# Optimization experiments

Measured on AMD Instinct MI355X. Metric: run time of the kernel, lower is better.

The kernel has to match this reference:

```python
import jax, jax.numpy as jnp
import numpy as np

B, IH, IW, C = 128, 16, 16, 1024   # weighted_context NHWC; idf = IH*IW = 256
S, EMB, IDF = 32, 256, 256


def setup_inputs() -> dict:
    key = jax.random.key(0)
    k1, k2, k3 = jax.random.split(key, 3)
    return {
        "weighted_context": jax.random.normal(k1, (B, IH, IW, C), dtype=jnp.float32),
        "word_emb": jax.random.normal(k2, (B, S, EMB), dtype=jnp.float32),
        "conv_kernel": jax.random.normal(k3, (EMB, IDF), dtype=jnp.float32) * (1.0 / np.sqrt(EMB)),
        "conv_bias": jnp.zeros((IDF,), dtype=jnp.float32),
    }


def reference(weighted_context, word_emb, conv_kernel, conv_bias):
    b, ih, iw, c = weighted_context.shape
    s = word_emb.shape[1]
    # 1x1 conv over the (expanded) word embeddings == per-token linear projection
    we = jnp.einsum("bse,ei->bsi", word_emb, conv_kernel) + conv_bias  # [B, S, idf]
    wc = weighted_context.reshape(b, ih * iw, c)                        # [B, HW, C]
    # matmul(wc, we, transpose_a=True, transpose_b=True): contracts HW with idf (idf == HW)
    attn = jnp.einsum("bpc,bsp->bcs", wc, we)                           # [B, C, S]
    # reshape to [B*C, S] + softmax == softmax over last axis
    attn = jax.nn.softmax(attn, axis=-1)
    # matmul(we^T [B, idf, S], attn^T [B, S, C]) -> [B, idf, C]
    out = jnp.einsum("bsp,bcs->bpc", we, attn).reshape(b, ih, iw, c)
    return (out, attn)
```

## Files before the change

kernel.cpp:

```cpp
#include <hip/hip_runtime.h>


typedef float  f32x4  __attribute__((ext_vector_type(4)));
typedef short  bf16x8 __attribute__((ext_vector_type(8)));

namespace {
constexpr int kB = 128, kHW = 256, kC = 1024, kS = 32, kE = 256;
constexpr int TP = kHW + 8;
constexpr int WR = kS + 8;
}

__device__ inline ushort f2bf(float x) {
  unsigned u = __float_as_uint(x);
  u += 0x7fffu + ((u >> 16) & 1u);
  return (ushort)(u >> 16);
}
__device__ inline float bf2f(ushort h) { return __uint_as_float(((unsigned)h) << 16); }

#define MFMA16(A, Bf, Cv) __builtin_amdgcn_mfma_f32_16x16x32_bf16((A), (Bf), (Cv), 0, 0, 0)

__global__ __launch_bounds__(256, 2) void fused_attn_kernel(
    const float* __restrict__ wc, const float* __restrict__ emb,
    const float* __restrict__ Km, const float* __restrict__ bias,
    float* __restrict__ out, float* __restrict__ attn_out) {
  const int b    = blockIdx.y;
  const int cb   = blockIdx.x * 256;
  const int tid  = threadIdx.x;
  const int wave = tid >> 6, lane = tid & 63;
  const int lr   = lane & 15, lg = lane >> 4;

  __shared__ ushort wHT[kS][TP];
  __shared__ ushort wLT[kS][TP];
  __shared__ ushort wHp[kHW][WR];
  __shared__ ushort pHl[kHW][WR];

  const float* wcb = wc + (size_t)b * kHW * kC;
  const int c0 = cb + wave * 64;

  float avC[8], avN[8];
#pragma unroll
  for (int i = 0; i < 8; ++i)
    avC[i] = wcb[(size_t)(lg * 8 + i) * kC + c0 + lr];

  {
    const float* embb = emb + (size_t)b * kS * kE;
    f32x4 pcc[2][4];
#pragma unroll
    for (int m = 0; m < 2; ++m)
#pragma unroll
      for (int n = 0; n < 4; ++n) pcc[m][n] = (f32x4){0.f, 0.f, 0.f, 0.f};

#pragma unroll 1
    for (int kt = 0; kt < 8; ++kt) {
      bf16x8 eah[2], eal[2];
#pragma unroll
      for (int m = 0; m < 2; ++m) {
        const float* ep = embb + (size_t)(m * 16 + lr) * kE + kt * 32 + lg * 8;
        const float4 v0 = *(const float4*)ep;
        const float4 v1 = *(const float4*)(ep + 4);
        const float ev[8] = {v0.x, v0.y, v0.z, v0.w, v1.x, v1.y, v1.z, v1.w};
#pragma unroll
        for (int i = 0; i < 8; ++i) {
          const ushort h = f2bf(ev[i]);
          eah[m][i] = (short)h;
          eal[m][i] = (short)f2bf(ev[i] - bf2f(h));
        }
      }
#pragma unroll
      for (int n = 0; n < 4; ++n) {
        const int pg = wave * 64 + n * 16 + lr;
        bf16x8 kh, kl;
#pragma unroll
        for (int i = 0; i < 8; ++i) {
          const float kv = Km[(size_t)(kt * 32 + lg * 8 + i) * kHW + pg];
          const ushort h = f2bf(kv);
          kh[i] = (short)h;
          kl[i] = (short)f2bf(kv - bf2f(h));
        }
#pragma unroll
        for (int m = 0; m < 2; ++m) {
          pcc[m][n] = MFMA16(eah[m], kh, pcc[m][n]);
          pcc[m][n] = MFMA16(eah[m], kl, pcc[m][n]);
          pcc[m][n] = MFMA16(eal[m], kh, pcc[m][n]);
        }
      }
    }
#pragma unroll
    for (int n = 0; n < 4; ++n) {
      const int pg = wave * 64 + n * 16 + lr;
      const float bv = bias[pg];
#pragma unroll
      for (int m = 0; m < 2; ++m)
#pragma unroll
        for (int j = 0; j < 4; ++j) {
          const float x = pcc[m][n][j] + bv;
          const ushort h = f2bf(x);
          const ushort l = f2bf(x - bf2f(h));
          const int s = m * 16 + lg * 4 + j;
          wHT[s][pg] = h;
          wLT[s][pg] = l;
          wHp[pg][s] = h;
        }
    }
  }
  __syncthreads();

  f32x4 acc[4][2];
#pragma unroll
  for (int m = 0; m < 4; ++m)
#pragma unroll
    for (int n = 0; n < 2; ++n) acc[m][n] = (f32x4){0.f, 0.f, 0.f, 0.f};

#pragma unroll 1
  for (int kt = 0; kt < 8; ++kt) {
    bf16x8 bh[2], bl[2];
#pragma unroll
    for (int n = 0; n < 2; ++n) {
      bh[n] = *(const bf16x8*)&wHT[n * 16 + lr][kt * 32 + lg * 8];
      bl[n] = *(const bf16x8*)&wLT[n * 16 + lr][kt * 32 + lg * 8];
    }
#pragma unroll
    for (int m = 0; m < 4; ++m) {
      const int mn  = (m + 1) & 3;
      const int ktn = (m == 3) ? kt + 1 : kt;
      if (!(kt == 7 && m == 3)) {
#pragma unroll
        for (int i = 0; i < 8; ++i)
          avN[i] = wcb[(size_t)(ktn * 32 + lg * 8 + i) * kC + c0 + mn * 16 + lr];
      }
      bf16x8 ah, al;
#pragma unroll
      for (int i = 0; i < 8; ++i) {
        const ushort h = f2bf(avC[i]);
        ah[i] = (short)h;
        al[i] = (short)f2bf(avC[i] - bf2f(h));
      }
#pragma unroll
      for (int n = 0; n < 2; ++n) {
        acc[m][n] = MFMA16(ah, bh[n], acc[m][n]);
        acc[m][n] = MFMA16(ah, bl[n], acc[m][n]);
        acc[m][n] = MFMA16(al, bh[n], acc[m][n]);
      }
#pragma unroll
      for (int i = 0; i < 8; ++i) avC[i] = avN[i];
    }
  }

  float* attnb = attn_out + ((size_t)b * kC + cb) * kS;
#pragma unroll
  for (int m = 0; m < 4; ++m) {
#pragma unroll
    for (int j = 0; j < 4; ++j) {
      float v0 = acc[m][0][j], v1 = acc[m][1][j];
      float mx = fmaxf(v0, v1);
      mx = fmaxf(mx, __shfl_xor(mx, 1));
      mx = fmaxf(mx, __shfl_xor(mx, 2));
      mx = fmaxf(mx, __shfl_xor(mx, 4));
      mx = fmaxf(mx, __shfl_xor(mx, 8));
      float e0 = __expf(v0 - mx), e1 = __expf(v1 - mx);
      float sm = e0 + e1;
      sm += __shfl_xor(sm, 1); sm += __shfl_xor(sm, 2);
      sm += __shfl_xor(sm, 4); sm += __shfl_xor(sm, 8);
      const float inv = 1.f / sm;
      e0 *= inv; e1 *= inv;
      const int cL = wave * 64 + m * 16 + lg * 4 + j;
      attnb[(size_t)cL * kS + lr]      = e0;
      attnb[(size_t)cL * kS + 16 + lr] = e1;
      pHl[cL][lr]      = f2bf(e0);
      pHl[cL][16 + lr] = f2bf(e1);
    }
  }

  bf16x8 pbh[4];
#pragma unroll
  for (int n = 0; n < 4; ++n)
    pbh[n] = *(const bf16x8*)&pHl[wave * 64 + n * 16 + lr][lg * 8];

  float* outb = out + (size_t)b * kHW * kC + cb;
#pragma unroll 1
  for (int pt = 0; pt < 16; ++pt) {
    const bf16x8 ah = *(const bf16x8*)&wHp[pt * 16 + lr][lg * 8];
#pragma unroll
    for (int n = 0; n < 4; ++n) {
      f32x4 o = (f32x4){0.f, 0.f, 0.f, 0.f};
      o = MFMA16(ah, pbh[n], o);
      const int ccol = wave * 64 + n * 16 + lr;
#pragma unroll
      for (int j = 0; j < 4; ++j)
        outb[(size_t)(pt * 16 + lg * 4 + j) * kC + ccol] = o[j];
    }
  }
}

extern "C" void kernel_launch(void* const* d_in, const int* in_sizes, int n_in,
                              void* d_out, int out_size, void* d_ws, size_t ws_size,
                              hipStream_t stream) {
  const float* wc   = (const float*)d_in[0];
  const float* emb  = (const float*)d_in[1];
  const float* Km   = (const float*)d_in[2];
  const float* bias = (const float*)d_in[3];

  float* out  = (float*)d_out;
  float* attn = out + (size_t)kB * kHW * kC;

  fused_attn_kernel<<<dim3(4, kB), 256, 0, stream>>>(wc, emb, Km, bias, out, attn);
}
```

Before: 83.21 us.

## Pre-split conv kernel to bf16 hi/lo, double waves per block, restructure output GEMM

Adds a small prep kernel that converts the conv weight into transposed bf16 high/low halves in workspace, so the fused kernel stops reconverting the same weights in every block. The fused kernel now runs 512 threads (8 waves) per block, and each wave owns 32 positions and 32 channels, which halves per-wave register tiles and raises occupancy. The embedding and weight loads are software-prefetched a step ahead. The final out GEMM is reorganised so each wave writes its own rows of positions across all channels, using softmax probabilities shared through LDS after a new barrier. The cost is an extra launch, a workspace round trip, and an additional block-wide sync.

```diff
diff --git a/kernel.cpp b/kernel.cpp
--- a/kernel.cpp
+++ b/kernel.cpp
@@ -19,10 +19,21 @@
 
 #define MFMA16(A, Bf, Cv) __builtin_amdgcn_mfma_f32_16x16x32_bf16((A), (Bf), (Cv), 0, 0, 0)
 
-__global__ __launch_bounds__(256, 2) void fused_attn_kernel(
+__global__ __launch_bounds__(256) void km_prep_kernel(
+    const float* __restrict__ Km, ushort* __restrict__ kh,
+    ushort* __restrict__ kl) {
+  const int p = blockIdx.x, e = threadIdx.x;
+  const float v = Km[(size_t)e * kHW + p];
+  const ushort h = f2bf(v);
+  kh[(size_t)p * kE + e] = h;
+  kl[(size_t)p * kE + e] = (ushort)f2bf(v - bf2f(h));
+}
+
+__global__ __launch_bounds__(512, 4) void fused_attn_kernel(
     const float* __restrict__ wc, const float* __restrict__ emb,
-    const float* __restrict__ Km, const float* __restrict__ bias,
-    float* __restrict__ out, float* __restrict__ attn_out) {
+    const ushort* __restrict__ kmh, const ushort* __restrict__ kml,
+    const float* __restrict__ bias, float* __restrict__ out,
+    float* __restrict__ attn_out) {
   const int b    = blockIdx.y;
   const int cb   = blockIdx.x * 256;
   const int tid  = threadIdx.x;
@@ -35,30 +46,53 @@
   __shared__ ushort pHl[kHW][WR];
 
   const float* wcb = wc + (size_t)b * kHW * kC;
-  const int c0 = cb + wave * 64;
-
-  float avC[8], avN[8];
-#pragma unroll
-  for (int i = 0; i < 8; ++i)
-    avC[i] = wcb[(size_t)(lg * 8 + i) * kC + c0 + lr];
+  const int c0 = cb + wave * 32;
+  const int p0 = wave * 32;
 
   {
     const float* embb = emb + (size_t)b * kS * kE;
-    f32x4 pcc[2][4];
+    f32x4 pcc[2][2];
 #pragma unroll
     for (int m = 0; m < 2; ++m)
 #pragma unroll
-      for (int n = 0; n < 4; ++n) pcc[m][n] = (f32x4){0.f, 0.f, 0.f, 0.f};
+      for (int n = 0; n < 2; ++n) pcc[m][n] = (f32x4){0.f, 0.f, 0.f, 0.f};
+
+    float4 eC[2][2]; bf16x8 khC[2], klC[2];
+#pragma unroll
+    for (int m = 0; m < 2; ++m) {
+      const float* ep = embb + (size_t)(m * 16 + lr) * kE + lg * 8;
+      eC[m][0] = *(const float4*)ep;
+      eC[m][1] = *(const float4*)(ep + 4);
+    }
+#pragma unroll
+    for (int n = 0; n < 2; ++n) {
+      const int pg = p0 + n * 16 + lr;
+      khC[n] = *(const bf16x8*)&kmh[(size_t)pg * kE + lg * 8];
+      klC[n] = *(const bf16x8*)&kml[(size_t)pg * kE + lg * 8];
+    }
 
 #pragma unroll 1
     for (int kt = 0; kt < 8; ++kt) {
+      float4 eN[2][2]; bf16x8 khN[2], klN[2];
+      if (kt < 7) {
+        const int ko = (kt + 1) * 32;
+#pragma unroll
+        for (int m = 0; m < 2; ++m) {
+          const float* ep = embb + (size_t)(m * 16 + lr) * kE + ko + lg * 8;
+          eN[m][0] = *(const float4*)ep;
+          eN[m][1] = *(const float4*)(ep + 4);
+        }
+#pragma unroll
+        for (int n = 0; n < 2; ++n) {
+          const int pg = p0 + n * 16 + lr;
+          khN[n] = *(const bf16x8*)&kmh[(size_t)pg * kE + ko + lg * 8];
+          klN[n] = *(const bf16x8*)&kml[(size_t)pg * kE + ko + lg * 8];
+        }
+      }
       bf16x8 eah[2], eal[2];
 #pragma unroll
       for (int m = 0; m < 2; ++m) {
-        const float* ep = embb + (size_t)(m * 16 + lr) * kE + kt * 32 + lg * 8;
-        const float4 v0 = *(const float4*)ep;
-        const float4 v1 = *(const float4*)(ep + 4);
-        const float ev[8] = {v0.x, v0.y, v0.z, v0.w, v1.x, v1.y, v1.z, v1.w};
+        const float* ev = (const float*)&eC[m][0];
 #pragma unroll
         for (int i = 0; i < 8; ++i) {
           const ushort h = f2bf(ev[i]);
@@ -67,27 +101,23 @@
         }
       }
 #pragma unroll
-      for (int n = 0; n < 4; ++n) {
-        const int pg = wave * 64 + n * 16 + lr;
-        bf16x8 kh, kl;
-#pragma unroll
-        for (int i = 0; i < 8; ++i) {
-          const float kv = Km[(size_t)(kt * 32 + lg * 8 + i) * kHW + pg];
-          const ushort h = f2bf(kv);
-          kh[i] = (short)h;
-          kl[i] = (short)f2bf(kv - bf2f(h));
-        }
+      for (int n = 0; n < 2; ++n)
 #pragma unroll
         for (int m = 0; m < 2; ++m) {
-          pcc[m][n] = MFMA16(eah[m], kh, pcc[m][n]);
-          pcc[m][n] = MFMA16(eah[m], kl, pcc[m][n]);
-          pcc[m][n] = MFMA16(eal[m], kh, pcc[m][n]);
-        }
-      }
-    }
-#pragma unroll
-    for (int n = 0; n < 4; ++n) {
-      const int pg = wave * 64 + n * 16 + lr;
+          pcc[m][n] = MFMA16(eah[m], khC[n], pcc[m][n]);
+          pcc[m][n] = MFMA16(eah[m], klC[n], pcc[m][n]);
+          pcc[m][n] = MFMA16(eal[m], khC[n], pcc[m][n]);
+        }
+      if (kt < 7) {
+#pragma unroll
+        for (int m = 0; m < 2; ++m) { eC[m][0] = eN[m][0]; eC[m][1] = eN[m][1]; }
+#pragma unroll
+        for (int n = 0; n < 2; ++n) { khC[n] = khN[n]; klC[n] = klN[n]; }
+      }
+    }
+#pragma unroll
+    for (int n = 0; n < 2; ++n) {
+      const int pg = p0 + n * 16 + lr;
       const float bv = bias[pg];
 #pragma unroll
       for (int m = 0; m < 2; ++m)
@@ -95,19 +125,26 @@
         for (int j = 0; j < 4; ++j) {
           const float x = pcc[m][n][j] + bv;
           const ushort h = f2bf(x);
-          const ushort l = f2bf(x - bf2f(h));
           const int s = m * 16 + lg * 4 + j;
           wHT[s][pg] = h;
-          wLT[s][pg] = l;
+          wLT[s][pg] = (ushort)f2bf(x - bf2f(h));
           wHp[pg][s] = h;
         }
     }
   }
+
+  float avC[2][8], avN[2][8];
+#pragma unroll
+  for (int m = 0; m < 2; ++m)
+#pragma unroll
+    for (int i = 0; i < 8; ++i)
+      avC[m][i] = wcb[(size_t)(lg * 8 + i) * kC + c0 + m * 16 + lr];
+
   __syncthreads();
 
-  f32x4 acc[4][2];
-#pragma unroll
-  for (int m = 0; m < 4; ++m)
+  f32x4 acc[2][2];
+#pragma unroll
+  for (int m = 0; m < 2; ++m)
 #pragma unroll
     for (int n = 0; n < 2; ++n) acc[m][n] = (f32x4){0.f, 0.f, 0.f, 0.f};
 
@@ -119,21 +156,21 @@
       bh[n] = *(const bf16x8*)&wHT[n * 16 + lr][kt * 32 + lg * 8];
       bl[n] = *(const bf16x8*)&wLT[n * 16 + lr][kt * 32 + lg * 8];
     }
-#pragma unroll
-    for (int m = 0; m < 4; ++m) {
-      const int mn  = (m + 1) & 3;
-      const int ktn = (m == 3) ? kt + 1 : kt;
-      if (!(kt == 7 && m == 3)) {
+    if (kt < 7) {
+#pragma unroll
+      for (int m = 0; m < 2; ++m)
 #pragma unroll
         for (int i = 0; i < 8; ++i)
-          avN[i] = wcb[(size_t)(ktn * 32 + lg * 8 + i) * kC + c0 + mn * 16 + lr];
-      }
+          avN[m][i] = wcb[(size_t)((kt + 1) * 32 + lg * 8 + i) * kC + c0 + m * 16 + lr];
+    }
+#pragma unroll
+    for (int m = 0; m < 2; ++m) {
       bf16x8 ah, al;
 #pragma unroll
       for (int i = 0; i < 8; ++i) {
-        const ushort h = f2bf(avC[i]);
+        const ushort h = f2bf(avC[m][i]);
         ah[i] = (short)h;
-        al[i] = (short)f2bf(avC[i] - bf2f(h));
+        al[i] = (short)f2bf(avC[m][i] - bf2f(h));
       }
 #pragma unroll
       for (int n = 0; n < 2; ++n) {
@@ -141,14 +178,18 @@
         acc[m][n] = MFMA16(ah, bl[n], acc[m][n]);
         acc[m][n] = MFMA16(al, bh[n], acc[m][n]);
       }
-#pragma unroll
-      for (int i = 0; i < 8; ++i) avC[i] = avN[i];
+    }
+    if (kt < 7) {
+#pragma unroll
+      for (int m = 0; m < 2; ++m)
+#pragma unroll
+        for (int i = 0; i < 8; ++i) avC[m][i] = avN[m][i];
     }
   }
 
   float* attnb = attn_out + ((size_t)b * kC + cb) * kS;
 #pragma unroll
-  for (int m = 0; m < 4; ++m) {
+  for (int m = 0; m < 2; ++m) {
 #pragma unroll
     for (int j = 0; j < 4; ++j) {
       float v0 = acc[m][0][j], v1 = acc[m][1][j];
@@ -163,32 +204,35 @@
       sm += __shfl_xor(sm, 4); sm += __shfl_xor(sm, 8);
       const float inv = 1.f / sm;
       e0 *= inv; e1 *= inv;
-      const int cL = wave * 64 + m * 16 + lg * 4 + j;
+      const int cL = wave * 32 + m * 16 + lg * 4 + j;
       attnb[(size_t)cL * kS + lr]      = e0;
       attnb[(size_t)cL * kS + 16 + lr] = e1;
       pHl[cL][lr]      = f2bf(e0);
       pHl[cL][16 + lr] = f2bf(e1);
     }
   }
-
-  bf16x8 pbh[4];
-#pragma unroll
-  for (int n = 0; n < 4; ++n)
-    pbh[n] = *(const bf16x8*)&pHl[wave * 64 + n * 16 + lr][lg * 8];
-
+  __syncthreads();
+
+  const bf16x8 ahB0 = *(const bf16x8*)&wHp[p0 + lr][lg * 8];
+  const bf16x8 ahB1 = *(const bf16x8*)&wHp[p0 + 16 + lr][lg * 8];
   float* outb = out + (size_t)b * kHW * kC + cb;
+
+  bf16x8 pbC = *(const bf16x8*)&pHl[lr][lg * 8];
 #pragma unroll 1
-  for (int pt = 0; pt < 16; ++pt) {
-    const bf16x8 ah = *(const bf16x8*)&wHp[pt * 16 + lr][lg * 8];
-#pragma unroll
-    for (int n = 0; n < 4; ++n) {
-      f32x4 o = (f32x4){0.f, 0.f, 0.f, 0.f};
-      o = MFMA16(ah, pbh[n], o);
-      const int ccol = wave * 64 + n * 16 + lr;
-#pragma unroll
-      for (int j = 0; j < 4; ++j)
-        outb[(size_t)(pt * 16 + lg * 4 + j) * kC + ccol] = o[j];
-    }
+  for (int ct = 0; ct < 16; ++ct) {
+    bf16x8 pbN;
+    if (ct < 15) pbN = *(const bf16x8*)&pHl[(ct + 1) * 16 + lr][lg * 8];
+    f32x4 o0 = (f32x4){0.f, 0.f, 0.f, 0.f};
+    f32x4 o1 = (f32x4){0.f, 0.f, 0.f, 0.f};
+    o0 = MFMA16(ahB0, pbC, o0);
+    o1 = MFMA16(ahB1, pbC, o1);
+    const int ccol = ct * 16 + lr;
+#pragma unroll
+    for (int j = 0; j < 4; ++j) {
+      outb[(size_t)(p0 + lg * 4 + j) * kC + ccol]      = o0[j];
+      outb[(size_t)(p0 + 16 + lg * 4 + j) * kC + ccol] = o1[j];
+    }
+    pbC = pbN;
   }
 }
 
@@ -202,6 +246,10 @@
 
   float* out  = (float*)d_out;
   float* attn = out + (size_t)kB * kHW * kC;
-
-  fused_attn_kernel<<<dim3(4, kB), 256, 0, stream>>>(wc, emb, Km, bias, out, attn);
-}
+  ushort* kmh = (ushort*)d_ws;
+  ushort* kml = kmh + (size_t)kHW * kE;
+
+  km_prep_kernel<<<dim3(kHW), 256, 0, stream>>>(Km, kmh, kml);
+  fused_attn_kernel<<<dim3(4, kB), 512, 0, stream>>>(wc, emb, kmh, kml, bias,
+                                                     out, attn);
+}
```

Measured after the change: 94.23 us. 13.2% more time.

## Restructure per-column-tile pipeline with full-tile prefetch and interleaved output

Applied to the files above, without the earlier changes.

The loop nest is reordered so each wave handles one 16-column tile at a time. It computes the scores, softmax and output projection for that tile before moving to the next, and prefetches the whole next tile of weighted_context (64 floats per lane) into a double-buffered register array. The goal is to overlap global loads of the next tile and output stores with compute, and to drop the 8-tile accumulator array. In exchange, register pressure rises sharply (128 floats of prefetch buffer), which may cause spills or lower occupancy under launch_bounds(256,2), and the B operands in LDS are reread for every tile.

```diff
diff --git a/kernel.cpp b/kernel.cpp
--- a/kernel.cpp
+++ b/kernel.cpp
@@ -37,10 +37,12 @@
   const float* wcb = wc + (size_t)b * kHW * kC;
   const int c0 = cb + wave * 64;
 
-  float avC[8], avN[8];
+  float w[2][64];
 #pragma unroll
-  for (int i = 0; i < 8; ++i)
-    avC[i] = wcb[(size_t)(lg * 8 + i) * kC + c0 + lr];
+  for (int kt = 0; kt < 8; ++kt)
+#pragma unroll
+    for (int i = 0; i < 8; ++i)
+      w[0][kt * 8 + i] = wcb[(size_t)(kt * 32 + lg * 8 + i) * kC + c0 + lr];
 
   {
     const float* embb = emb + (size_t)b * kS * kE;
@@ -95,63 +97,58 @@
         for (int j = 0; j < 4; ++j) {
           const float x = pcc[m][n][j] + bv;
           const ushort h = f2bf(x);
-          const ushort l = f2bf(x - bf2f(h));
           const int s = m * 16 + lg * 4 + j;
           wHT[s][pg] = h;
-          wLT[s][pg] = l;
+          wLT[s][pg] = (ushort)f2bf(x - bf2f(h));
           wHp[pg][s] = h;
         }
     }
   }
   __syncthreads();
 
-  f32x4 acc[4][2];
+  float* attnb = attn_out + ((size_t)b * kC + cb) * kS;
+  float* outb  = out + (size_t)b * kHW * kC + cb;
+
 #pragma unroll
-  for (int m = 0; m < 4; ++m)
+  for (int m = 0; m < 4; ++m) {
+    const int cur = m & 1, nxt = cur ^ 1;
+
+    if (m < 3) {
 #pragma unroll
-    for (int n = 0; n < 2; ++n) acc[m][n] = (f32x4){0.f, 0.f, 0.f, 0.f};
-
-#pragma unroll 1
-  for (int kt = 0; kt < 8; ++kt) {
-    bf16x8 bh[2], bl[2];
-#pragma unroll
-    for (int n = 0; n < 2; ++n) {
-      bh[n] = *(const bf16x8*)&wHT[n * 16 + lr][kt * 32 + lg * 8];
-      bl[n] = *(const bf16x8*)&wLT[n * 16 + lr][kt * 32 + lg * 8];
-    }
-#pragma unroll
-    for (int m = 0; m < 4; ++m) {
-      const int mn  = (m + 1) & 3;
-      const int ktn = (m == 3) ? kt + 1 : kt;
-      if (!(kt == 7 && m == 3)) {
+      for (int kt = 0; kt < 8; ++kt)
 #pragma unroll
         for (int i = 0; i < 8; ++i)
-          avN[i] = wcb[(size_t)(ktn * 32 + lg * 8 + i) * kC + c0 + mn * 16 + lr];
-      }
+          w[nxt][kt * 8 + i] =
+              wcb[(size_t)(kt * 32 + lg * 8 + i) * kC + c0 + (m + 1) * 16 + lr];
+    }
+
+    f32x4 acc0 = (f32x4){0.f, 0.f, 0.f, 0.f};
+    f32x4 acc1 = (f32x4){0.f, 0.f, 0.f, 0.f};
+#pragma unroll
+    for (int kt = 0; kt < 8; ++kt) {
+      const bf16x8 bh0 = *(const bf16x8*)&wHT[lr][kt * 32 + lg * 8];
+      const bf16x8 bl0 = *(const bf16x8*)&wLT[lr][kt * 32 + lg * 8];
+      const bf16x8 bh1 = *(const bf16x8*)&wHT[16 + lr][kt * 32 + lg * 8];
+      const bf16x8 bl1 = *(const bf16x8*)&wLT[16 + lr][kt * 32 + lg * 8];
       bf16x8 ah, al;
 #pragma unroll
       for (int i = 0; i < 8; ++i) {
-        const ushort h = f2bf(avC[i]);
+        const float v = w[cur][kt * 8 + i];
+        const ushort h = f2bf(v);
         ah[i] = (short)h;
-        al[i] = (short)f2bf(avC[i] - bf2f(h));
+        al[i] = (short)f2bf(v - bf2f(h));
       }
-#pragma unroll
-      for (int n = 0; n < 2; ++n) {
-        acc[m][n] = MFMA16(ah, bh[n], acc[m][n]);
-        acc[m][n] = MFMA16(ah, bl[n], acc[m][n]);
-        acc[m][n] = MFMA16(al, bh[n], acc[m][n]);
-      }
-#pragma unroll
-      for (int i = 0; i < 8; ++i) avC[i] = avN[i];
+      acc0 = MFMA16(ah, bh0, acc0);
+      acc0 = MFMA16(ah, bl0, acc0);
+      acc0 = MFMA16(al, bh0, acc0);
+      acc1 = MFMA16(ah, bh1, acc1);
+      acc1 = MFMA16(ah, bl1, acc1);
+      acc1 = MFMA16(al, bh1, acc1);
     }
-  }
 
-  float* attnb = attn_out + ((size_t)b * kC + cb) * kS;
-#pragma unroll
-  for (int m = 0; m < 4; ++m) {
 #pragma unroll
     for (int j = 0; j < 4; ++j) {
-      float v0 = acc[m][0][j], v1 = acc[m][1][j];
+      float v0 = acc0[j], v1 = acc1[j];
       float mx = fmaxf(v0, v1);
       mx = fmaxf(mx, __shfl_xor(mx, 1));
       mx = fmaxf(mx, __shfl_xor(mx, 2));
@@ -169,22 +166,14 @@
       pHl[cL][lr]      = f2bf(e0);
       pHl[cL][16 + lr] = f2bf(e1);
     }
-  }
 
-  bf16x8 pbh[4];
-#pragma unroll
-  for (int n = 0; n < 4; ++n)
-    pbh[n] = *(const bf16x8*)&pHl[wave * 64 + n * 16 + lr][lg * 8];
-
-  float* outb = out + (size_t)b * kHW * kC + cb;
+    const bf16x8 pb = *(const bf16x8*)&pHl[wave * 64 + m * 16 + lr][lg * 8];
+    const int ccol = wave * 64 + m * 16 + lr;
 #pragma unroll 1
-  for (int pt = 0; pt < 16; ++pt) {
-    const bf16x8 ah = *(const bf16x8*)&wHp[pt * 16 + lr][lg * 8];
-#pragma unroll
-    for (int n = 0; n < 4; ++n) {
+    for (int pt = 0; pt < 16; ++pt) {
+      const bf16x8 ah = *(const bf16x8*)&wHp[pt * 16 + lr][lg * 8];
       f32x4 o = (f32x4){0.f, 0.f, 0.f, 0.f};
-      o = MFMA16(ah, pbh[n], o);
-      const int ccol = wave * 64 + n * 16 + lr;
+      o = MFMA16(ah, pb, o);
 #pragma unroll
       for (int j = 0; j < 4; ++j)
         outb[(size_t)(pt * 16 + lg * 4 + j) * kC + ccol] = o[j];
```

New measurement: 141.8 us. 1.7x slower.
